# Kernel optimization log

Measured on AMD Instinct MI355X. Metric: run time of the kernel, lower is better.

Reference implementation:

```python
import jax, jax.numpy as jnp
import numpy as np

TOP_K = 2  # num_experts_per_tok


def setup_inputs() -> dict:
    key = jax.random.key(0)
    ks = jax.random.split(key, 4)
    B, S, H, I, E = 4, 2048, 2048, 4096, 8
    std = 0.02
    hidden_states = jax.random.normal(ks[0], (B, S, H), dtype=jnp.float32)
    gate_w = jax.random.normal(ks[1], (E, H), dtype=jnp.float32) * std   # nn.Linear weight [E,H]
    wfc = jax.random.normal(ks[2], (E, I, H), dtype=jnp.float32) * std   # c_fc weight [E,out,in]
    bfc = jnp.zeros((E, I), dtype=jnp.float32)                           # bias zero-init
    wproj = jax.random.normal(ks[3], (E, H, I), dtype=jnp.float32) * std # c_proj weight
    bproj = jnp.zeros((E, H), dtype=jnp.float32)
    return {"hidden_states": hidden_states, "gate_w": gate_w, "wfc": wfc,
            "bfc": bfc, "wproj": wproj, "bproj": bproj}


def reference(hidden_states, gate_w, wfc, bfc, wproj, bproj):
    B, S, H = hidden_states.shape
    E = wfc.shape[0]
    x = hidden_states.reshape(-1, H)                      # [T, H]
    router_logits = x @ gate_w.T                          # [T, E]
    top_vals, top_idx = jax.lax.top_k(router_logits, TOP_K)
    router_weights = jax.nn.softmax(top_vals.astype(jnp.float32), axis=-1).astype(x.dtype)  # [T, k]
    out = jnp.zeros_like(x)
    # Loop over the small fixed set of experts; each token contributes with its
    # combined gate weight for that expert (0 if not routed there). Same math as
    # the torch gather/grouped-GEMM/scatter-add path.
    for e in range(E):
        gate_e = jnp.sum(jnp.where(top_idx == e, router_weights, 0.0), axis=-1)  # [T]
        h = jax.nn.gelu(x @ wfc[e].T + bfc[e], approximate=False)                # [T, I]
        y = h @ wproj[e].T + bproj[e]                                            # [T, H]
        out = out + gate_e[:, None] * y
    return out.reshape(B, S, H), router_logits
```

## Files before the change

kernel.cpp:

```cpp
#include <hip/hip_runtime.h>
#include <hip/hip_bf16.h>
#include <math.h>

#define NT 8192
#define HD 2048
#define ID 4096
#define NE 8
#define MAXSLOT 17408
#define MAXRB 136

typedef __bf16 bf16x8 __attribute__((ext_vector_type(8)));
typedef float f32x4 __attribute__((ext_vector_type(4)));

__device__ __forceinline__ float bf2f(unsigned short u){
  union{unsigned u; float f;} v; v.u = ((unsigned)u) << 16; return v.f;
}

#define GLDS0(g, l) __builtin_amdgcn_global_load_lds( \
    (const __attribute__((address_space(1))) void*)(g), \
    (__attribute__((address_space(3))) void*)(l), 16, 0, 0)

__global__ __launch_bounds__(256) void cvt_kernel(const float* __restrict__ in,
                                                  __hip_bfloat16* __restrict__ outp, int n4){
  int i = blockIdx.x * blockDim.x + threadIdx.x;
  int stride = gridDim.x * blockDim.x;
  for (; i < n4; i += stride){
    float4 v = reinterpret_cast<const float4*>(in)[i];
    union{ushort4 u; __hip_bfloat16 h[4];} o;
    o.h[0] = __float2bfloat16(v.x); o.h[1] = __float2bfloat16(v.y);
    o.h[2] = __float2bfloat16(v.z); o.h[3] = __float2bfloat16(v.w);
    reinterpret_cast<ushort4*>(outp)[i] = o.u;
  }
}

__global__ __launch_bounds__(256) void cvt_dual_kernel(
    const float* __restrict__ in0, __hip_bfloat16* __restrict__ out0, int n4_0,
    const float* __restrict__ in1, __hip_bfloat16* __restrict__ out1, int n4_1)
{
  int i = blockIdx.x * blockDim.x + threadIdx.x;
  int stride = gridDim.x * blockDim.x;
  const int total = n4_0 + n4_1;
  for (; i < total; i += stride){
    const float* src; __hip_bfloat16* dst; int j;
    if (i < n4_0){ src = in0; dst = out0; j = i; }
    else         { src = in1; dst = out1; j = i - n4_0; }
    float4 v = reinterpret_cast<const float4*>(src)[j];
    union{ushort4 u; __hip_bfloat16 h[4];} o;
    o.h[0] = __float2bfloat16(v.x); o.h[1] = __float2bfloat16(v.y);
    o.h[2] = __float2bfloat16(v.z); o.h[3] = __float2bfloat16(v.w);
    reinterpret_cast<ushort4*>(dst)[j] = o.u;
  }
}

__global__ __launch_bounds__(256) void router_kernel(
    const float* __restrict__ x, const float* __restrict__ gw,
    float* __restrict__ logits_out, int* __restrict__ tokExp,
    float* __restrict__ tokW, int* __restrict__ cnt)
{
  int wave = (blockIdx.x * blockDim.x + threadIdx.x) >> 6;
  int lane = threadIdx.x & 63;
  if (wave >= NT) return;
  const float* xr = x + (long)wave * HD;
  double acc[NE];
  #pragma unroll
  for (int e = 0; e < NE; e++) acc[e] = 0.0;
  for (int k = lane; k < HD; k += 64){
    double xv = (double)xr[k];
    #pragma unroll
    for (int e = 0; e < NE; e++) acc[e] += xv * (double)gw[e * HD + k];
  }
  #pragma unroll
  for (int e = 0; e < NE; e++){
    #pragma unroll
    for (int off = 32; off; off >>= 1) acc[e] += __shfl_down(acc[e], off, 64);
  }
  if (lane == 0){
    int e0 = 0; double v0 = acc[0];
    for (int e = 1; e < NE; e++) if (acc[e] > v0){ v0 = acc[e]; e0 = e; }
    int e1 = -1; double v1 = -1e300;
    for (int e = 0; e < NE; e++) if (e != e0 && acc[e] > v1){ v1 = acc[e]; e1 = e; }
    double ex = exp(v1 - v0);
    double s = 1.0 + ex;
    for (int e = 0; e < NE; e++) logits_out[wave * NE + e] = (float)acc[e];
    tokExp[wave * 2]     = e0; tokExp[wave * 2 + 1] = e1;
    tokW[wave * 2]       = (float)(1.0 / s);
    tokW[wave * 2 + 1]   = (float)(ex / s);
    atomicAdd(&cnt[e0], 1); atomicAdd(&cnt[e1], 1);
  }
}

__global__ void offsets_kernel(const int* __restrict__ cnt, int* __restrict__ padOff){
  if (threadIdx.x == 0 && blockIdx.x == 0){
    int o = 0;
    for (int e = 0; e < NE; e++){ padOff[e] = o; o += ((cnt[e] + 127) >> 7) << 7; }
    padOff[NE] = o;
  }
}

__global__ __launch_bounds__(256) void scatter_kernel(
    const int* __restrict__ tokExp, const float* __restrict__ tokW,
    const int* __restrict__ padOff, int* cursor,
    int* __restrict__ slotTok, int* __restrict__ tokSlot)
{
  int t = blockIdx.x * blockDim.x + threadIdx.x;
  if (t >= NT) return;
  #pragma unroll
  for (int s = 0; s < 2; s++){
    int e = tokExp[t * 2 + s];
    int pos = atomicAdd(&cursor[e], 1);
    int slot = padOff[e] + pos;
    slotTok[slot] = t;
    tokSlot[t * 2 + s] = slot;
  }
}

template<int GATHER_A, int EPI, int ND, int KD>
__global__ __launch_bounds__(256, 3) void moe_gemm_v12(
    const __hip_bfloat16* __restrict__ A,
    const __hip_bfloat16* __restrict__ W,
    const float* __restrict__ bias,
    const int* __restrict__ slotTok,
    const int* __restrict__ padOff,
    __hip_bfloat16* __restrict__ Yout)
{
  __shared__ __align__(16) __hip_bfloat16 lds[3 * 8192];
  const int rb = blockIdx.y;
  if (rb * 128 >= padOff[NE]) return;
  const int cb = blockIdx.x;
  int e = 0;
  #pragma unroll
  for (int i = 1; i < NE; i++) if (rb * 128 >= padOff[i]) e = i;

  const int tid  = threadIdx.x;
  const int lane = tid & 63;
  const int w    = tid >> 6;
  const int wr   = w >> 1, wc = w & 1;

  const int r16s = lane >> 2;
  const int cgs  = (lane & 3) ^ ((r16s >> 1) & 3);
  long aRow0, aRow1;
  {
    int g0 = rb * 128 + 32 * w + r16s, g1 = g0 + 16;
    if (GATHER_A){
      int t0 = slotTok[g0]; if (t0 < 0) t0 = 0;
      int t1 = slotTok[g1]; if (t1 < 0) t1 = 0;
      aRow0 = t0; aRow1 = t1;
    } else { aRow0 = g0; aRow1 = g1; }
  }
  const __hip_bfloat16* sA0 = A + aRow0 * (long)KD + cgs * 8;
  const __hip_bfloat16* sA1 = A + aRow1 * (long)KD + cgs * 8;
  const long bRow0 = (long)cb * 128 + 32 * w + r16s;
  const __hip_bfloat16* sB0 = W + (long)e * ND * KD + bRow0 * KD + cgs * 8;
  const __hip_bfloat16* sB1 = sB0 + 16 * (long)KD;

  __hip_bfloat16* dst0 = &lds[0 * 8192 + 2 * w * 512];
  __hip_bfloat16* dst1 = &lds[1 * 8192 + 2 * w * 512];
  __hip_bfloat16* dst2 = &lds[2 * 8192 + 2 * w * 512];

  const int r16f  = lane & 15;
  const int laneF = r16f * 32 + (((lane >> 4) ^ ((r16f >> 1) & 3))) * 8;
  const int adrA  = wr * 2048 + laneF;
  const int adrB  = 4096 + wc * 2048 + laneF;

  f32x4 acc[4][4] = {};

  constexpr int NKS = KD / 32;

#define STGADV(DP) do{ \
    GLDS0(sA0, (DP)); GLDS0(sA1, (DP) + 512); \
    GLDS0(sB0, (DP) + 4096); GLDS0(sB1, (DP) + 4096 + 512); \
    sA0 += 32; sA1 += 32; sB0 += 32; sB1 += 32; \
    asm volatile("" : "+v"(sA0), "+v"(sA1), "+v"(sB0), "+v"(sB1)); \
  }while(0)

#define RD_A(BUFC, M) (*reinterpret_cast<const bf16x8*>(&lds[(BUFC)*8192 + (M)*512 + adrA]))
#define RD_B(BUFC, N) (*reinterpret_cast<const bf16x8*>(&lds[(BUFC)*8192 + (N)*512 + adrB]))

#define BODY(K, BUFC, DP_STG) do{ \
    const int tt = t + (K); \
    if (tt < NKS){ \
      const bool dost = (tt + 2 < NKS); \
      if (dost){ STGADV(DP_STG); } \
      bf16x8 a0 = RD_A(BUFC,0), a1 = RD_A(BUFC,1), a2 = RD_A(BUFC,2), a3 = RD_A(BUFC,3); \
      bf16x8 b0 = RD_B(BUFC,0), b1 = RD_B(BUFC,1), b2 = RD_B(BUFC,2), b3 = RD_B(BUFC,3); \
      __builtin_amdgcn_s_setprio(1); \
      acc[0][0] = __builtin_amdgcn_mfma_f32_16x16x32_bf16(a0, b0, acc[0][0],0,0,0); \
      acc[1][0] = __builtin_amdgcn_mfma_f32_16x16x32_bf16(a1, b0, acc[1][0],0,0,0); \
      acc[2][0] = __builtin_amdgcn_mfma_f32_16x16x32_bf16(a2, b0, acc[2][0],0,0,0); \
      acc[3][0] = __builtin_amdgcn_mfma_f32_16x16x32_bf16(a3, b0, acc[3][0],0,0,0); \
      acc[0][1] = __builtin_amdgcn_mfma_f32_16x16x32_bf16(a0, b1, acc[0][1],0,0,0); \
      acc[1][1] = __builtin_amdgcn_mfma_f32_16x16x32_bf16(a1, b1, acc[1][1],0,0,0); \
      acc[2][1] = __builtin_amdgcn_mfma_f32_16x16x32_bf16(a2, b1, acc[2][1],0,0,0); \
      acc[3][1] = __builtin_amdgcn_mfma_f32_16x16x32_bf16(a3, b1, acc[3][1],0,0,0); \
      acc[0][2] = __builtin_amdgcn_mfma_f32_16x16x32_bf16(a0, b2, acc[0][2],0,0,0); \
      acc[1][2] = __builtin_amdgcn_mfma_f32_16x16x32_bf16(a1, b2, acc[1][2],0,0,0); \
      acc[2][2] = __builtin_amdgcn_mfma_f32_16x16x32_bf16(a2, b2, acc[2][2],0,0,0); \
      acc[3][2] = __builtin_amdgcn_mfma_f32_16x16x32_bf16(a3, b2, acc[3][2],0,0,0); \
      acc[0][3] = __builtin_amdgcn_mfma_f32_16x16x32_bf16(a0, b3, acc[0][3],0,0,0); \
      acc[1][3] = __builtin_amdgcn_mfma_f32_16x16x32_bf16(a1, b3, acc[1][3],0,0,0); \
      acc[2][3] = __builtin_amdgcn_mfma_f32_16x16x32_bf16(a2, b3, acc[2][3],0,0,0); \
      acc[3][3] = __builtin_amdgcn_mfma_f32_16x16x32_bf16(a3, b3, acc[3][3],0,0,0); \
      __builtin_amdgcn_s_setprio(0); \
      if (dost) asm volatile("s_waitcnt vmcnt(4)" ::: "memory"); \
      else      asm volatile("s_waitcnt vmcnt(0)" ::: "memory"); \
      __builtin_amdgcn_s_barrier(); \
    } \
  }while(0)

  STGADV(dst0);
  STGADV(dst1);
  asm volatile("s_waitcnt vmcnt(4)" ::: "memory");
  __builtin_amdgcn_s_barrier();

  for (int t = 0; t < NKS; t += 3){
    BODY(0, 0, dst2);
    BODY(1, 1, dst0);
    BODY(2, 2, dst1);
  }

  const int col0 = cb * 128 + wc * 64 + (lane & 15);
  const int row0 = rb * 128 + wr * 64 + (lane >> 4) * 4;
  #pragma unroll
  for (int n = 0; n < 4; n++){
    const int col = col0 + n * 16;
    const float bb = bias[(long)e * ND + col];
    #pragma unroll
    for (int m = 0; m < 4; m++){
      const long rbase = (long)(row0 + m * 16);
      #pragma unroll
      for (int r = 0; r < 4; r++){
        float v = acc[m][n][r] + bb;
        if (EPI == 0){
          float u = 0.7978845608f * (v + 0.044715f * v * v * v);
          float t2 = 1.0f - 2.0f / (__expf(2.0f * u) + 1.0f);
          v = 0.5f * v * (1.0f + t2);
        }
        Yout[(rbase + r) * ND + col] = __float2bfloat16(v);
      }
    }
  }
#undef STGADV
#undef RD_A
#undef RD_B
#undef BODY
}

__global__ __launch_bounds__(256) void combine_kernel(
    const __hip_bfloat16* __restrict__ yb,
    const int* __restrict__ tokSlot, const float* __restrict__ tokW,
    float* __restrict__ outp)
{
  const int t  = blockIdx.x;
  const int c0 = threadIdx.x * 8;
  const int s0 = tokSlot[t * 2], s1 = tokSlot[t * 2 + 1];
  const float w0 = tokW[t * 2], w1 = tokW[t * 2 + 1];
  const ushort4* p0 = reinterpret_cast<const ushort4*>(yb + (long)s0 * HD + c0);
  const ushort4* p1 = reinterpret_cast<const ushort4*>(yb + (long)s1 * HD + c0);
  float4 o[2];
  #pragma unroll
  for (int h = 0; h < 2; h++){
    ushort4 a = p0[h], b = p1[h];
    o[h].x = w0 * bf2f(a.x) + w1 * bf2f(b.x);
    o[h].y = w0 * bf2f(a.y) + w1 * bf2f(b.y);
    o[h].z = w0 * bf2f(a.z) + w1 * bf2f(b.z);
    o[h].w = w0 * bf2f(a.w) + w1 * bf2f(b.w);
  }
  float4* po = reinterpret_cast<float4*>(outp + (long)t * HD + c0);
  po[0] = o[0]; po[1] = o[1];
}

extern "C" void kernel_launch(void* const* d_in, const int* in_sizes, int n_in,
                              void* d_out, int out_size, void* d_ws, size_t ws_size,
                              hipStream_t stream)
{
  (void)in_sizes; (void)n_in; (void)out_size;
  const float* x     = (const float*)d_in[0];
  const float* gw    = (const float*)d_in[1];
  const float* wfc   = (const float*)d_in[2];
  const float* bfc   = (const float*)d_in[3];
  const float* wproj = (const float*)d_in[4];
  const float* bproj = (const float*)d_in[5];
  float* outp   = (float*)d_out;
  float* logits = outp + (size_t)NT * HD;

  char* ws = (char*)d_ws;
  size_t off = 0;
  auto alloc = [&](size_t b){ void* p = ws + off; off += (b + 255) & ~(size_t)255; return p; };

  char* shared0 = (char*)alloc((size_t)MAXSLOT * HD * 2);
  __hip_bfloat16* xb = (__hip_bfloat16*)shared0;
  __hip_bfloat16* yb = (__hip_bfloat16*)shared0;
  __hip_bfloat16* hb = (__hip_bfloat16*)alloc((size_t)MAXSLOT * ID * 2);
  int*   slotTok = (int*)alloc(MAXSLOT * 4);
  int*   tokExp  = (int*)alloc(NT * 2 * 4);
  float* tokW    = (float*)alloc(NT * 2 * 4);
  int*   tokSlot = (int*)alloc(NT * 2 * 4);
  int*   meta    = (int*)alloc(256);
  int* cnt = meta; int* cursor = meta + 8; int* padOff = meta + 16;

  const size_t WB1 = (size_t)NE * ID * HD * 2;
  const bool dual = (off + 2 * WB1) <= ws_size;
  __hip_bfloat16* wBa = (__hip_bfloat16*)(ws + off);
  __hip_bfloat16* wBb = dual ? (__hip_bfloat16*)(ws + off + WB1) : wBa;

  hipMemsetAsync(meta, 0, 256, stream);
  hipMemsetAsync(slotTok, 0xFF, MAXSLOT * 4, stream);

  cvt_kernel<<<4096, 256, 0, stream>>>(x, xb, NT * HD / 4);
  router_kernel<<<NT / 4, 256, 0, stream>>>(x, gw, logits, tokExp, tokW, cnt);
  offsets_kernel<<<1, 64, 0, stream>>>(cnt, padOff);
  scatter_kernel<<<NT / 256, 256, 0, stream>>>(tokExp, tokW, padOff, cursor, slotTok, tokSlot);

  if (dual){
    cvt_dual_kernel<<<4096, 256, 0, stream>>>(wfc, wBa, NE * ID * HD / 4,
                                              wproj, wBb, NE * HD * ID / 4);
    moe_gemm_v12<1, 0, ID, HD><<<dim3(ID / 128, MAXRB), 256, 0, stream>>>(xb, wBa, bfc, slotTok, padOff, hb);
    moe_gemm_v12<0, 1, HD, ID><<<dim3(HD / 128, MAXRB), 256, 0, stream>>>(hb, wBb, bproj, slotTok, padOff, yb);
  } else {
    cvt_kernel<<<4096, 256, 0, stream>>>(wfc, wBa, NE * ID * HD / 4);
    moe_gemm_v12<1, 0, ID, HD><<<dim3(ID / 128, MAXRB), 256, 0, stream>>>(xb, wBa, bfc, slotTok, padOff, hb);
    cvt_kernel<<<4096, 256, 0, stream>>>(wproj, wBb, NE * HD * ID / 4);
    moe_gemm_v12<0, 1, HD, ID><<<dim3(HD / 128, MAXRB), 256, 0, stream>>>(hb, wBb, bproj, slotTok, padOff, yb);
  }

  combine_kernel<<<NT, 256, 0, stream>>>(yb, tokSlot, tokW, outp);
}
```

Before: 1.211 ms.

## Overlap wproj bf16 conversion with first expert GEMM via extra tail blocks

```diff
diff --git a/kernel.cpp b/kernel.cpp
--- a/kernel.cpp
+++ b/kernel.cpp
@@ -30,25 +30,6 @@
     o.h[0] = __float2bfloat16(v.x); o.h[1] = __float2bfloat16(v.y);
     o.h[2] = __float2bfloat16(v.z); o.h[3] = __float2bfloat16(v.w);
     reinterpret_cast<ushort4*>(outp)[i] = o.u;
-  }
-}
-
-__global__ __launch_bounds__(256) void cvt_dual_kernel(
-    const float* __restrict__ in0, __hip_bfloat16* __restrict__ out0, int n4_0,
-    const float* __restrict__ in1, __hip_bfloat16* __restrict__ out1, int n4_1)
-{
-  int i = blockIdx.x * blockDim.x + threadIdx.x;
-  int stride = gridDim.x * blockDim.x;
-  const int total = n4_0 + n4_1;
-  for (; i < total; i += stride){
-    const float* src; __hip_bfloat16* dst; int j;
-    if (i < n4_0){ src = in0; dst = out0; j = i; }
-    else         { src = in1; dst = out1; j = i - n4_0; }
-    float4 v = reinterpret_cast<const float4*>(src)[j];
-    union{ushort4 u; __hip_bfloat16 h[4];} o;
-    o.h[0] = __float2bfloat16(v.x); o.h[1] = __float2bfloat16(v.y);
-    o.h[2] = __float2bfloat16(v.z); o.h[3] = __float2bfloat16(v.w);
-    reinterpret_cast<ushort4*>(dst)[j] = o.u;
   }
 }
 
@@ -114,19 +95,41 @@
   }
 }
 
-template<int GATHER_A, int EPI, int ND, int KD>
+template<int GATHER_A, int EPI, int ND, int KD, int FUSE_CVT>
 __global__ __launch_bounds__(256, 3) void moe_gemm_v12(
     const __hip_bfloat16* __restrict__ A,
     const __hip_bfloat16* __restrict__ W,
     const float* __restrict__ bias,
     const int* __restrict__ slotTok,
     const int* __restrict__ padOff,
-    __hip_bfloat16* __restrict__ Yout)
+    __hip_bfloat16* __restrict__ Yout,
+    const float* __restrict__ cvIn,
+    __hip_bfloat16* __restrict__ cvOut)
 {
   __shared__ __align__(16) __hip_bfloat16 lds[3 * 8192];
-  const int rb = blockIdx.y;
+  constexpr int NCB = ND / 128;
+  constexpr int GEMM_BLKS = NCB * MAXRB;
+  int cb, rb;
+  if (FUSE_CVT){
+    const int bid = blockIdx.x;
+    if (bid >= GEMM_BLKS){
+      const int n4 = NE * ID * HD / 4;
+      int i = (bid - GEMM_BLKS) * 256 + (int)threadIdx.x;
+      const int stride = 4096 * 256;
+      for (; i < n4; i += stride){
+        float4 v = reinterpret_cast<const float4*>(cvIn)[i];
+        union{ushort4 u; __hip_bfloat16 h[4];} o;
+        o.h[0] = __float2bfloat16(v.x); o.h[1] = __float2bfloat16(v.y);
+        o.h[2] = __float2bfloat16(v.z); o.h[3] = __float2bfloat16(v.w);
+        reinterpret_cast<ushort4*>(cvOut)[i] = o.u;
+      }
+      return;
+    }
+    cb = bid % NCB; rb = bid / NCB;
+  } else {
+    cb = blockIdx.x; rb = blockIdx.y;
+  }
   if (rb * 128 >= padOff[NE]) return;
-  const int cb = blockIdx.x;
   int e = 0;
   #pragma unroll
   for (int i = 1; i < NE; i++) if (rb * 128 >= padOff[i]) e = i;
@@ -306,21 +309,24 @@
   hipMemsetAsync(meta, 0, 256, stream);
   hipMemsetAsync(slotTok, 0xFF, MAXSLOT * 4, stream);
 
-  cvt_kernel<<<4096, 256, 0, stream>>>(x, xb, NT * HD / 4);
+  cvt_kernel<<<2048, 256, 0, stream>>>(x, xb, NT * HD / 4);
   router_kernel<<<NT / 4, 256, 0, stream>>>(x, gw, logits, tokExp, tokW, cnt);
   offsets_kernel<<<1, 64, 0, stream>>>(cnt, padOff);
   scatter_kernel<<<NT / 256, 256, 0, stream>>>(tokExp, tokW, padOff, cursor, slotTok, tokSlot);
 
+  cvt_kernel<<<4096, 256, 0, stream>>>(wfc, wBa, NE * ID * HD / 4);
+
   if (dual){
-    cvt_dual_kernel<<<4096, 256, 0, stream>>>(wfc, wBa, NE * ID * HD / 4,
-                                              wproj, wBb, NE * HD * ID / 4);
-    moe_gemm_v12<1, 0, ID, HD><<<dim3(ID / 128, MAXRB), 256, 0, stream>>>(xb, wBa, bfc, slotTok, padOff, hb);
-    moe_gemm_v12<0, 1, HD, ID><<<dim3(HD / 128, MAXRB), 256, 0, stream>>>(hb, wBb, bproj, slotTok, padOff, yb);
+    moe_gemm_v12<1, 0, ID, HD, 1><<<(ID / 128) * MAXRB + 4096, 256, 0, stream>>>(
+        xb, wBa, bfc, slotTok, padOff, hb, wproj, wBb);
+    moe_gemm_v12<0, 1, HD, ID, 0><<<dim3(HD / 128, MAXRB), 256, 0, stream>>>(
+        hb, wBb, bproj, slotTok, padOff, yb, nullptr, nullptr);
   } else {
-    cvt_kernel<<<4096, 256, 0, stream>>>(wfc, wBa, NE * ID * HD / 4);
-    moe_gemm_v12<1, 0, ID, HD><<<dim3(ID / 128, MAXRB), 256, 0, stream>>>(xb, wBa, bfc, slotTok, padOff, hb);
+    moe_gemm_v12<1, 0, ID, HD, 0><<<dim3(ID / 128, MAXRB), 256, 0, stream>>>(
+        xb, wBa, bfc, slotTok, padOff, hb, nullptr, nullptr);
     cvt_kernel<<<4096, 256, 0, stream>>>(wproj, wBb, NE * HD * ID / 4);
-    moe_gemm_v12<0, 1, HD, ID><<<dim3(HD / 128, MAXRB), 256, 0, stream>>>(hb, wBb, bproj, slotTok, padOff, yb);
+    moe_gemm_v12<0, 1, HD, ID, 0><<<dim3(HD / 128, MAXRB), 256, 0, stream>>>(
+        hb, wBb, bproj, slotTok, padOff, yb, nullptr, nullptr);
   }
 
   combine_kernel<<<NT, 256, 0, stream>>>(yb, tokSlot, tokW, outp);
```

After: 1.191 ms (median of 2 runs). No clear change (-1.7%).
